# Kernel tuning notes

Measured on AMD Instinct MI355X. Metric: run time of the kernel, lower is better.

## Reference

```python
import jax, jax.numpy as jnp
import numpy as np

N_NODES = 100000
N_EDGES = 600000
D_FEAT = 128
N_OUT = 1


def setup_inputs() -> dict:
    key = jax.random.key(0)
    k1, k2, k3, k4 = jax.random.split(key, 4)
    node_inputs = jax.random.normal(k1, (N_NODES, D_FEAT), dtype=jnp.float32)
    r_indices = jax.random.randint(k2, (N_EDGES,), 0, N_NODES, dtype=jnp.int64)
    c_indices = jax.random.randint(k3, (N_EDGES,), 0, N_NODES, dtype=jnp.int64)
    w = jax.random.normal(k4, (D_FEAT, N_OUT), dtype=jnp.float32) * 0.05
    b = jnp.zeros((N_OUT,), dtype=jnp.float32)
    return {"node_inputs": node_inputs, "r_indices": r_indices,
            "c_indices": c_indices, "w": w, "b": b}


def reference(node_inputs, r_indices, c_indices, w, b):
    # Gather edge endpoints: [E, D]
    row_inputs = node_inputs[r_indices]
    col_inputs = node_inputs[c_indices]
    diff = jnp.abs(row_inputs - col_inputs)          # [E, D]
    out = diff @ w + b                               # [E, n_out]
    out = jnp.squeeze(out, axis=-1)                  # n_out == 1
    return out  # act is identity (default)
```

## Files before the change

kernel.cpp:

```cpp
#include <hip/hip_runtime.h>
#include <hip/hip_bf16.h>
#include <hip/hip_fp16.h>


#define D_FEAT 128

__global__ __launch_bounds__(256) void convert_f32_to_f16(
    const float* __restrict__ src, __half* __restrict__ dst, int n8)
{
    const int i = blockIdx.x * blockDim.x + threadIdx.x;
    if (i >= n8) return;
    const float4* s = (const float4*)src + 2 * (size_t)i;
    const float4 a = s[0];
    const float4 c = s[1];
    float4 packed;
    ((__half2*)&packed)[0] = __floats2half2_rn(a.x, a.y);
    ((__half2*)&packed)[1] = __floats2half2_rn(a.z, a.w);
    ((__half2*)&packed)[2] = __floats2half2_rn(c.x, c.y);
    ((__half2*)&packed)[3] = __floats2half2_rn(c.z, c.w);
    ((float4*)dst)[i] = packed;
}

__global__ __launch_bounds__(256) void gather_edges_f16_ilp(
    const __half* __restrict__ tbl,
    const int*   __restrict__ r_idx,
    const int*   __restrict__ c_idx,
    const float* __restrict__ w,
    const float* __restrict__ b,
    float*       __restrict__ out,
    int n_edges)
{
    const int tid  = blockIdx.x * blockDim.x + threadIdx.x;
    const int lane = tid & 7;
    const int edge = tid >> 3;
    if (edge >= n_edges) return;

    const int r = r_idx[edge];
    const int c = c_idx[edge];

    const float4* arow = (const float4*)(tbl + (size_t)r * D_FEAT);
    const float4* brow = (const float4*)(tbl + (size_t)c * D_FEAT);

    const float4 a0 = arow[lane];
    const float4 a1 = arow[lane + 8];
    const float4 b0 = brow[lane];
    const float4 b1 = brow[lane + 8];

    const float4 w00 = ((const float4*)w)[2 * lane + 0];
    const float4 w01 = ((const float4*)w)[2 * lane + 1];
    const float4 w10 = ((const float4*)w)[2 * lane + 16];
    const float4 w11 = ((const float4*)w)[2 * lane + 17];

    const __half2* a0h = (const __half2*)&a0;
    const __half2* b0h = (const __half2*)&b0;
    const __half2* a1h = (const __half2*)&a1;
    const __half2* b1h = (const __half2*)&b1;

    float s = 0.f;
    {
        const float2 x0 = __half22float2(a0h[0]), y0 = __half22float2(b0h[0]);
        const float2 x1 = __half22float2(a0h[1]), y1 = __half22float2(b0h[1]);
        const float2 x2 = __half22float2(a0h[2]), y2 = __half22float2(b0h[2]);
        const float2 x3 = __half22float2(a0h[3]), y3 = __half22float2(b0h[3]);
        s += fabsf(x0.x - y0.x) * w00.x + fabsf(x0.y - y0.y) * w00.y
           + fabsf(x1.x - y1.x) * w00.z + fabsf(x1.y - y1.y) * w00.w
           + fabsf(x2.x - y2.x) * w01.x + fabsf(x2.y - y2.y) * w01.y
           + fabsf(x3.x - y3.x) * w01.z + fabsf(x3.y - y3.y) * w01.w;
    }
    {
        const float2 x0 = __half22float2(a1h[0]), y0 = __half22float2(b1h[0]);
        const float2 x1 = __half22float2(a1h[1]), y1 = __half22float2(b1h[1]);
        const float2 x2 = __half22float2(a1h[2]), y2 = __half22float2(b1h[2]);
        const float2 x3 = __half22float2(a1h[3]), y3 = __half22float2(b1h[3]);
        s += fabsf(x0.x - y0.x) * w10.x + fabsf(x0.y - y0.y) * w10.y
           + fabsf(x1.x - y1.x) * w10.z + fabsf(x1.y - y1.y) * w10.w
           + fabsf(x2.x - y2.x) * w11.x + fabsf(x2.y - y2.y) * w11.y
           + fabsf(x3.x - y3.x) * w11.z + fabsf(x3.y - y3.y) * w11.w;
    }

    #pragma unroll
    for (int off = 4; off > 0; off >>= 1)
        s += __shfl_xor(s, off, 64);

    if (lane == 0)
        out[edge] = s + b[0];
}

__global__ __launch_bounds__(256) void gather_edges_f32(
    const float* __restrict__ nodes,
    const int*   __restrict__ r_idx,
    const int*   __restrict__ c_idx,
    const float* __restrict__ w,
    const float* __restrict__ b,
    float*       __restrict__ out,
    int n_edges)
{
    const int tid  = blockIdx.x * blockDim.x + threadIdx.x;
    const int lane = tid & 31;
    const int edge = tid >> 5;
    if (edge >= n_edges) return;

    const int r = r_idx[edge];
    const int c = c_idx[edge];

    const float4 wv = ((const float4*)w)[lane];
    const float4 av = ((const float4*)(nodes + (size_t)r * D_FEAT))[lane];
    const float4 bv = ((const float4*)(nodes + (size_t)c * D_FEAT))[lane];

    float s = fabsf(av.x - bv.x) * wv.x
            + fabsf(av.y - bv.y) * wv.y
            + fabsf(av.z - bv.z) * wv.z
            + fabsf(av.w - bv.w) * wv.w;

    #pragma unroll
    for (int off = 16; off > 0; off >>= 1)
        s += __shfl_xor(s, off, 64);

    if (lane == 0)
        out[edge] = s + b[0];
}

extern "C" void kernel_launch(void* const* d_in, const int* in_sizes, int n_in,
                              void* d_out, int out_size, void* d_ws, size_t ws_size,
                              hipStream_t stream) {
    const float* nodes = (const float*)d_in[0];
    const int*   r_idx = (const int*)d_in[1];
    const int*   c_idx = (const int*)d_in[2];
    const float* w     = (const float*)d_in[3];
    const float* b     = (const float*)d_in[4];
    float*       out   = (float*)d_out;

    const int n_edges   = in_sizes[1];
    const int n_nodes_f = in_sizes[0];
    const size_t tbl_bytes = (size_t)n_nodes_f * sizeof(__half);

    if (ws_size >= tbl_bytes && (n_nodes_f & 7) == 0) {
        __half* tbl = (__half*)d_ws;

        const int n8 = n_nodes_f / 8;
        const int cblock = 256;
        const int cgrid  = (n8 + cblock - 1) / cblock;
        convert_f32_to_f16<<<cgrid, cblock, 0, stream>>>(nodes, tbl, n8);

        const int block = 256;
        const int grid  = (n_edges * 8 + block - 1) / block;
        gather_edges_f16_ilp<<<grid, block, 0, stream>>>(
            tbl, r_idx, c_idx, w, b, out, n_edges);
    } else {
        const int block = 256;
        const int grid  = (n_edges * 32 + block - 1) / block;
        gather_edges_f32<<<grid, block, 0, stream>>>(
            nodes, r_idx, c_idx, w, b, out, n_edges);
    }
}
```

Baseline: 131.1 us.

## Use packed fp16 fdot2 with fp16 weights and four lanes per edge

Converts the weight vector to fp16 inside the existing conversion kernel. The edge kernel now computes the difference in packed half2 arithmetic, clears the sign bits to take the absolute value, and accumulates with the fdot2 intrinsic into fp32. Each edge is handled by four threads instead of eight, with each thread loading four 16-byte chunks per row. This cuts ALU work and per-edge thread count, but doing the subtraction in fp16 and using fp16 weights loses some precision.

```diff
diff --git a/kernel.cpp b/kernel.cpp
--- a/kernel.cpp
+++ b/kernel.cpp
@@ -1,14 +1,31 @@
 #include <hip/hip_runtime.h>
 #include <hip/hip_bf16.h>
 #include <hip/hip_fp16.h>
+#include <stdint.h>
 
 
 #define D_FEAT 128
 
+typedef _Float16 h2v __attribute__((ext_vector_type(2)));
+
 __global__ __launch_bounds__(256) void convert_f32_to_f16(
-    const float* __restrict__ src, __half* __restrict__ dst, int n8)
+    const float* __restrict__ src, __half* __restrict__ dst,
+    const float* __restrict__ w, __half* __restrict__ wh, int n8)
 {
     const int i = blockIdx.x * blockDim.x + threadIdx.x;
+
+    if (blockIdx.x == 0 && threadIdx.x < (D_FEAT / 8)) {
+        const float4* s = (const float4*)w + 2 * (size_t)threadIdx.x;
+        const float4 a = s[0];
+        const float4 c = s[1];
+        float4 packed;
+        ((__half2*)&packed)[0] = __floats2half2_rn(a.x, a.y);
+        ((__half2*)&packed)[1] = __floats2half2_rn(a.z, a.w);
+        ((__half2*)&packed)[2] = __floats2half2_rn(c.x, c.y);
+        ((__half2*)&packed)[3] = __floats2half2_rn(c.z, c.w);
+        ((float4*)wh)[threadIdx.x] = packed;
+    }
+
     if (i >= n8) return;
     const float4* s = (const float4*)src + 2 * (size_t)i;
     const float4 a = s[0];
@@ -21,66 +38,84 @@
     ((float4*)dst)[i] = packed;
 }
 
-__global__ __launch_bounds__(256) void gather_edges_f16_ilp(
+__device__ __forceinline__ float absdot(uint32_t a, uint32_t b, uint32_t w,
+                                        float acc)
+{
+#if __has_builtin(__builtin_amdgcn_fdot2)
+    const h2v av = __builtin_bit_cast(h2v, a);
+    const h2v bv = __builtin_bit_cast(h2v, b);
+    const h2v d  = av - bv;
+    const uint32_t ad = __builtin_bit_cast(uint32_t, d) & 0x7FFF7FFFu;
+    return __builtin_amdgcn_fdot2(__builtin_bit_cast(h2v, ad),
+                                  __builtin_bit_cast(h2v, w), acc, false);
+#else
+    const float2 x = __half22float2(__builtin_bit_cast(__half2, a));
+    const float2 y = __half22float2(__builtin_bit_cast(__half2, b));
+    const float2 ww = __half22float2(__builtin_bit_cast(__half2, w));
+    return acc + fabsf(x.x - y.x) * ww.x + fabsf(x.y - y.y) * ww.y;
+#endif
+}
+
+__global__ __launch_bounds__(256) void gather_edges_f16_dot(
     const __half* __restrict__ tbl,
+    const __half* __restrict__ wh,
     const int*   __restrict__ r_idx,
     const int*   __restrict__ c_idx,
-    const float* __restrict__ w,
     const float* __restrict__ b,
     float*       __restrict__ out,
     int n_edges)
 {
     const int tid  = blockIdx.x * blockDim.x + threadIdx.x;
-    const int lane = tid & 7;
-    const int edge = tid >> 3;
+    const int lane = tid & 3;
+    const int edge = tid >> 2;
     if (edge >= n_edges) return;
 
     const int r = r_idx[edge];
     const int c = c_idx[edge];
 
-    const float4* arow = (const float4*)(tbl + (size_t)r * D_FEAT);
-    const float4* brow = (const float4*)(tbl + (size_t)c * D_FEAT);
+    const uint4* arow = (const uint4*)(tbl + (size_t)r * D_FEAT);
+    const uint4* brow = (const uint4*)(tbl + (size_t)c * D_FEAT);
 
-    const float4 a0 = arow[lane];
-    const float4 a1 = arow[lane + 8];
-    const float4 b0 = brow[lane];
-    const float4 b1 = brow[lane + 8];
+    const uint4 a0 = arow[lane];
+    const uint4 a1 = arow[lane + 4];
+    const uint4 a2 = arow[lane + 8];
+    const uint4 a3 = arow[lane + 12];
+    const uint4 b0 = brow[lane];
+    const uint4 b1 = brow[lane + 4];
+    const uint4 b2 = brow[lane + 8];
+    const uint4 b3 = brow[lane + 12];
 
-    const float4 w00 = ((const float4*)w)[2 * lane + 0];
-    const float4 w01 = ((const float4*)w)[2 * lane + 1];
-    const float4 w10 = ((const float4*)w)[2 * lane + 16];
-    const float4 w11 = ((const float4*)w)[2 * lane + 17];
+    const uint4* wv = (const uint4*)wh;
+    const uint4 w0 = wv[lane];
+    const uint4 w1 = wv[lane + 4];
+    const uint4 w2 = wv[lane + 8];
+    const uint4 w3 = wv[lane + 12];
 
-    const __half2* a0h = (const __half2*)&a0;
-    const __half2* b0h = (const __half2*)&b0;
-    const __half2* a1h = (const __half2*)&a1;
-    const __half2* b1h = (const __half2*)&b1;
+    float s0 = 0.f, s1 = 0.f, s2 = 0.f, s3 = 0.f;
+    s0 = absdot(a0.x, b0.x, w0.x, s0);
+    s0 = absdot(a0.y, b0.y, w0.y, s0);
+    s0 = absdot(a0.z, b0.z, w0.z, s0);
+    s0 = absdot(a0.w, b0.w, w0.w, s0);
 
-    float s = 0.f;
-    {
-        const float2 x0 = __half22float2(a0h[0]), y0 = __half22float2(b0h[0]);
-        const float2 x1 = __half22float2(a0h[1]), y1 = __half22float2(b0h[1]);
-        const float2 x2 = __half22float2(a0h[2]), y2 = __half22float2(b0h[2]);
-        const float2 x3 = __half22float2(a0h[3]), y3 = __half22float2(b0h[3]);
-        s += fabsf(x0.x - y0.x) * w00.x + fabsf(x0.y - y0.y) * w00.y
-           + fabsf(x1.x - y1.x) * w00.z + fabsf(x1.y - y1.y) * w00.w
-           + fabsf(x2.x - y2.x) * w01.x + fabsf(x2.y - y2.y) * w01.y
-           + fabsf(x3.x - y3.x) * w01.z + fabsf(x3.y - y3.y) * w01.w;
-    }
-    {
-        const float2 x0 = __half22float2(a1h[0]), y0 = __half22float2(b1h[0]);
-        const float2 x1 = __half22float2(a1h[1]), y1 = __half22float2(b1h[1]);
-        const float2 x2 = __half22float2(a1h[2]), y2 = __half22float2(b1h[2]);
-        const float2 x3 = __half22float2(a1h[3]), y3 = __half22float2(b1h[3]);
-        s += fabsf(x0.x - y0.x) * w10.x + fabsf(x0.y - y0.y) * w10.y
-           + fabsf(x1.x - y1.x) * w10.z + fabsf(x1.y - y1.y) * w10.w
-           + fabsf(x2.x - y2.x) * w11.x + fabsf(x2.y - y2.y) * w11.y
-           + fabsf(x3.x - y3.x) * w11.z + fabsf(x3.y - y3.y) * w11.w;
-    }
+    s1 = absdot(a1.x, b1.x, w1.x, s1);
+    s1 = absdot(a1.y, b1.y, w1.y, s1);
+    s1 = absdot(a1.z, b1.z, w1.z, s1);
+    s1 = absdot(a1.w, b1.w, w1.w, s1);
 
-    #pragma unroll
-    for (int off = 4; off > 0; off >>= 1)
-        s += __shfl_xor(s, off, 64);
+    s2 = absdot(a2.x, b2.x, w2.x, s2);
+    s2 = absdot(a2.y, b2.y, w2.y, s2);
+    s2 = absdot(a2.z, b2.z, w2.z, s2);
+    s2 = absdot(a2.w, b2.w, w2.w, s2);
+
+    s3 = absdot(a3.x, b3.x, w3.x, s3);
+    s3 = absdot(a3.y, b3.y, w3.y, s3);
+    s3 = absdot(a3.z, b3.z, w3.z, s3);
+    s3 = absdot(a3.w, b3.w, w3.w, s3);
+
+    float s = (s0 + s1) + (s2 + s3);
+
+    s += __shfl_xor(s, 2, 64);
+    s += __shfl_xor(s, 1, 64);
 
     if (lane == 0)
         out[edge] = s + b[0];
@@ -133,22 +168,24 @@
     const int n_edges   = in_sizes[1];
     const int n_nodes_f = in_sizes[0];
     const size_t tbl_bytes = (size_t)n_nodes_f * sizeof(__half);
+    const size_t wh_bytes  = (size_t)D_FEAT * sizeof(__half);
 
-    if (ws_size >= tbl_bytes && (n_nodes_f & 7) == 0) {
+    if (ws_size >= tbl_bytes + wh_bytes && (n_nodes_f & 7) == 0) {
         __half* tbl = (__half*)d_ws;
+        __half* wh  = tbl + (size_t)n_nodes_f;
 
         const int n8 = n_nodes_f / 8;
         const int cblock = 256;
         const int cgrid  = (n8 + cblock - 1) / cblock;
-        convert_f32_to_f16<<<cgrid, cblock, 0, stream>>>(nodes, tbl, n8);
+        convert_f32_to_f16<<<cgrid, cblock, 0, stream>>>(nodes, tbl, w, wh, n8);
 
         const int block = 256;
-        const int grid  = (n_edges * 8 + block - 1) / block;
-        gather_edges_f16_ilp<<<grid, block, 0, stream>>>(
-            tbl, r_idx, c_idx, w, b, out, n_edges);
+        const int grid  = (int)(((long long)n_edges * 4 + block - 1) / block);
+        gather_edges_f16_dot<<<grid, block, 0, stream>>>(
+            tbl, wh, r_idx, c_idx, b, out, n_edges);
     } else {
         const int block = 256;
-        const int grid  = (n_edges * 32 + block - 1) / block;
+        const int grid  = (int)(((long long)n_edges * 32 + block - 1) / block);
         gather_edges_f32<<<grid, block, 0, stream>>>(
             nodes, r_idx, c_idx, w, b, out, n_edges);
     }
```

After: 130.2 us. About the same (-0.7%).

## Replace fp16 table conversion with feature-striped fp32 gather plus partial-sum reduce

Applied to the files above, without the earlier changes.

Drops the per-call fp32-to-fp16 conversion of the node table and instead splits the 128 features into four 32-feature stripes. Each block handles one stripe for 64 edges, with each lane group working on two edges at once, and writes per-stripe partial dot products to workspace. A second kernel sums the four stripes and adds the bias. The intent is to avoid rewriting the whole table each call and to keep each stripe's working set (about 12.8MB) resident in cache. The cost is a second launch, partial-sum traffic through workspace, and four index loads per edge.

```diff
diff --git a/kernel.cpp b/kernel.cpp
--- a/kernel.cpp
+++ b/kernel.cpp
@@ -1,89 +1,89 @@
 #include <hip/hip_runtime.h>
 #include <hip/hip_bf16.h>
 #include <hip/hip_fp16.h>
+#include <stdint.h>
 
 
-#define D_FEAT 128
+#define D_FEAT   128
+#define NSTRIPE  4
+#define DPS      32
+#define SLANES   8
+#define EPB      64
 
-__global__ __launch_bounds__(256) void convert_f32_to_f16(
-    const float* __restrict__ src, __half* __restrict__ dst, int n8)
-{
-    const int i = blockIdx.x * blockDim.x + threadIdx.x;
-    if (i >= n8) return;
-    const float4* s = (const float4*)src + 2 * (size_t)i;
-    const float4 a = s[0];
-    const float4 c = s[1];
-    float4 packed;
-    ((__half2*)&packed)[0] = __floats2half2_rn(a.x, a.y);
-    ((__half2*)&packed)[1] = __floats2half2_rn(a.z, a.w);
-    ((__half2*)&packed)[2] = __floats2half2_rn(c.x, c.y);
-    ((__half2*)&packed)[3] = __floats2half2_rn(c.z, c.w);
-    ((float4*)dst)[i] = packed;
-}
-
-__global__ __launch_bounds__(256) void gather_edges_f16_ilp(
-    const __half* __restrict__ tbl,
+__global__ __launch_bounds__(256) void k_gather_stripe(
+    const float* __restrict__ nodes,
     const int*   __restrict__ r_idx,
     const int*   __restrict__ c_idx,
     const float* __restrict__ w,
-    const float* __restrict__ b,
-    float*       __restrict__ out,
+    float*       __restrict__ partial,
     int n_edges)
 {
-    const int tid  = blockIdx.x * blockDim.x + threadIdx.x;
-    const int lane = tid & 7;
-    const int edge = tid >> 3;
-    if (edge >= n_edges) return;
+    const int kb = blockIdx.x & (NSTRIPE - 1);
+    const int bc = blockIdx.x >> 2;
+    const int l  = threadIdx.x & (SLANES - 1);
+    const int g  = threadIdx.x >> 3;
 
-    const int r = r_idx[edge];
-    const int c = c_idx[edge];
+    const float* sbase = nodes + kb * DPS;
+    const float4 wv = *(const float4*)(w + kb * DPS + l * 4);
+    float* pslice = partial + (size_t)kb * n_edges;
 
-    const float4* arow = (const float4*)(tbl + (size_t)r * D_FEAT);
-    const float4* brow = (const float4*)(tbl + (size_t)c * D_FEAT);
+    const int eA = bc * EPB + g;
+    const int eB = eA + 32;
+    const bool vA = eA < n_edges;
+    const bool vB = eB < n_edges;
 
-    const float4 a0 = arow[lane];
-    const float4 a1 = arow[lane + 8];
-    const float4 b0 = brow[lane];
-    const float4 b1 = brow[lane + 8];
+    const int rA = vA ? r_idx[eA] : 0;
+    const int cA = vA ? c_idx[eA] : 0;
+    const int rB = vB ? r_idx[eB] : 0;
+    const int cB = vB ? c_idx[eB] : 0;
 
-    const float4 w00 = ((const float4*)w)[2 * lane + 0];
-    const float4 w01 = ((const float4*)w)[2 * lane + 1];
-    const float4 w10 = ((const float4*)w)[2 * lane + 16];
-    const float4 w11 = ((const float4*)w)[2 * lane + 17];
+    const float4 aA = *(const float4*)(sbase + (size_t)rA * D_FEAT + l * 4);
+    const float4 bA = *(const float4*)(sbase + (size_t)cA * D_FEAT + l * 4);
+    const float4 aB = *(const float4*)(sbase + (size_t)rB * D_FEAT + l * 4);
+    const float4 bB = *(const float4*)(sbase + (size_t)cB * D_FEAT + l * 4);
 
-    const __half2* a0h = (const __half2*)&a0;
-    const __half2* b0h = (const __half2*)&b0;
-    const __half2* a1h = (const __half2*)&a1;
-    const __half2* b1h = (const __half2*)&b1;
+    float sA = fabsf(aA.x - bA.x) * wv.x + fabsf(aA.y - bA.y) * wv.y
+             + fabsf(aA.z - bA.z) * wv.z + fabsf(aA.w - bA.w) * wv.w;
+    float sB = fabsf(aB.x - bB.x) * wv.x + fabsf(aB.y - bB.y) * wv.y
+             + fabsf(aB.z - bB.z) * wv.z + fabsf(aB.w - bB.w) * wv.w;
 
-    float s = 0.f;
-    {
-        const float2 x0 = __half22float2(a0h[0]), y0 = __half22float2(b0h[0]);
-        const float2 x1 = __half22float2(a0h[1]), y1 = __half22float2(b0h[1]);
-        const float2 x2 = __half22float2(a0h[2]), y2 = __half22float2(b0h[2]);
-        const float2 x3 = __half22float2(a0h[3]), y3 = __half22float2(b0h[3]);
-        s += fabsf(x0.x - y0.x) * w00.x + fabsf(x0.y - y0.y) * w00.y
-           + fabsf(x1.x - y1.x) * w00.z + fabsf(x1.y - y1.y) * w00.w
-           + fabsf(x2.x - y2.x) * w01.x + fabsf(x2.y - y2.y) * w01.y
-           + fabsf(x3.x - y3.x) * w01.z + fabsf(x3.y - y3.y) * w01.w;
-    }
-    {
-        const float2 x0 = __half22float2(a1h[0]), y0 = __half22float2(b1h[0]);
-        const float2 x1 = __half22float2(a1h[1]), y1 = __half22float2(b1h[1]);
-        const float2 x2 = __half22float2(a1h[2]), y2 = __half22float2(b1h[2]);
-        const float2 x3 = __half22float2(a1h[3]), y3 = __half22float2(b1h[3]);
-        s += fabsf(x0.x - y0.x) * w10.x + fabsf(x0.y - y0.y) * w10.y
-           + fabsf(x1.x - y1.x) * w10.z + fabsf(x1.y - y1.y) * w10.w
-           + fabsf(x2.x - y2.x) * w11.x + fabsf(x2.y - y2.y) * w11.y
-           + fabsf(x3.x - y3.x) * w11.z + fabsf(x3.y - y3.y) * w11.w;
+    #pragma unroll
+    for (int off = 4; off > 0; off >>= 1) {
+        sA += __shfl_xor(sA, off, 64);
+        sB += __shfl_xor(sB, off, 64);
     }
 
-    #pragma unroll
-    for (int off = 4; off > 0; off >>= 1)
-        s += __shfl_xor(s, off, 64);
+    if (l == 0) {
+        if (vA) pslice[eA] = sA;
+        if (vB) pslice[eB] = sB;
+    }
+}
 
-    if (lane == 0)
-        out[edge] = s + b[0];
+__global__ __launch_bounds__(256) void k_reduce(
+    const float* __restrict__ partial, const float* __restrict__ b,
+    float* __restrict__ out, int n_edges)
+{
+    const int q  = blockIdx.x * blockDim.x + threadIdx.x;
+    const int e0 = q * 4;
+    if (e0 >= n_edges) return;
+    const float bb = b[0];
+    if (e0 + 4 <= n_edges) {
+        float4 acc = make_float4(bb, bb, bb, bb);
+        #pragma unroll
+        for (int k = 0; k < NSTRIPE; ++k) {
+            const float4 p =
+                *(const float4*)(partial + (size_t)k * n_edges + e0);
+            acc.x += p.x; acc.y += p.y; acc.z += p.z; acc.w += p.w;
+        }
+        *(float4*)(out + e0) = acc;
+    } else {
+        for (int e = e0; e < n_edges; ++e) {
+            float acc = bb;
+            for (int k = 0; k < NSTRIPE; ++k)
+                acc += partial[(size_t)k * n_edges + e];
+            out[e] = acc;
+        }
+    }
 }
 
 __global__ __launch_bounds__(256) void gather_edges_f32(
@@ -130,25 +130,26 @@
     const float* b     = (const float*)d_in[4];
     float*       out   = (float*)d_out;
 
-    const int n_edges   = in_sizes[1];
-    const int n_nodes_f = in_sizes[0];
-    const size_t tbl_bytes = (size_t)n_nodes_f * sizeof(__half);
+    const int n_edges = in_sizes[1];
 
-    if (ws_size >= tbl_bytes && (n_nodes_f & 7) == 0) {
-        __half* tbl = (__half*)d_ws;
+    const size_t part_bytes = (size_t)NSTRIPE * n_edges * sizeof(float);
 
-        const int n8 = n_nodes_f / 8;
-        const int cblock = 256;
-        const int cgrid  = (n8 + cblock - 1) / cblock;
-        convert_f32_to_f16<<<cgrid, cblock, 0, stream>>>(nodes, tbl, n8);
+    if (ws_size >= part_bytes) {
+        float* partial = (float*)d_ws;
 
-        const int block = 256;
-        const int grid  = (n_edges * 8 + block - 1) / block;
-        gather_edges_f16_ilp<<<grid, block, 0, stream>>>(
-            tbl, r_idx, c_idx, w, b, out, n_edges);
+        {
+            const int chunks = (n_edges + EPB - 1) / EPB;
+            k_gather_stripe<<<chunks * NSTRIPE, 256, 0, stream>>>(
+                nodes, r_idx, c_idx, w, partial, n_edges);
+        }
+        {
+            const int quads = (n_edges + 3) / 4;
+            const int grid  = (quads + 255) / 256;
+            k_reduce<<<grid, 256, 0, stream>>>(partial, b, out, n_edges);
+        }
     } else {
         const int block = 256;
-        const int grid  = (n_edges * 32 + block - 1) / block;
+        const int grid  = (int)(((long long)n_edges * 32 + block - 1) / block);
         gather_edges_f32<<<grid, block, 0, stream>>>(
             nodes, r_idx, c_idx, w, b, out, n_edges);
     }
```

Measured after the change: 152.8 us. 1.17x slower.
